# Kernel optimization log

Measured on AMD Instinct MI355X. Metric: run time of the kernel, lower is better.

Reference implementation:

```python
import jax, jax.numpy as jnp
import numpy as np

EPS = 1e-5
G = 8  # groups


def bn(x, gamma, beta):
    # BatchNorm2d in training mode: stats over (N, H, W) per channel (axis=1)
    m = jnp.mean(x, axis=(0, 2, 3), keepdims=True)
    v = jnp.var(x, axis=(0, 2, 3), keepdims=True)
    return (x - m) * jax.lax.rsqrt(v + EPS) * gamma.reshape(1, -1, 1, 1) + beta.reshape(1, -1, 1, 1)


def setup_inputs() -> dict:
    key = jax.random.key(0)
    ks = jax.random.split(key, 8)
    N, C, H, W = 8, 128, 56, 56
    Co = 128
    GP = Co // G  # 16 group planes
    d = {}
    d["x"] = jax.random.normal(ks[0], (N, C, H, W), jnp.float32)
    d["wq"] = jax.random.normal(ks[1], (Co // 2, C), jnp.float32) * np.float32(np.sqrt(1.0 / (C * GP)))
    d["wk"] = jax.random.normal(ks[2], (Co // 2, C), jnp.float32) * np.float32(np.sqrt(1.0 / C))
    d["wv"] = jax.random.normal(ks[3], (Co, C), jnp.float32) * np.float32(np.sqrt(1.0 / C))
    d["q_rel"] = jax.random.normal(ks[4], (GP // 2, H), jnp.float32) * np.float32(np.sqrt(1.0 / (Co // 2)))
    d["k_rel"] = jax.random.normal(ks[5], (GP // 2, H), jnp.float32) * np.float32(np.sqrt(1.0 / (Co // 2)))
    d["v_rel"] = jax.random.normal(ks[6], (GP, H), jnp.float32) * np.float32(np.sqrt(1.0 / Co))
    for name, n in [("q", Co // 2), ("k", Co // 2), ("v", Co), ("qr", G), ("kr", G), ("qk", G), ("sv", Co), ("sve", Co)]:
        d["g_" + name] = jnp.ones((n,), jnp.float32)
        d["b_" + name] = jnp.zeros((n,), jnp.float32)
    return d


def reference(x, wq, wk, wv, q_rel, k_rel, v_rel,
              g_q, b_q, g_k, b_k, g_v, b_v,
              g_qr, b_qr, g_kr, b_kr, g_qk, b_qk,
              g_sv, b_sv, g_sve, b_sve):
    N, C, H, W = x.shape
    # 1x1 conv transforms + BN
    q = bn(jnp.einsum('oc,bchw->bohw', wq, x), g_q, b_q)
    k = bn(jnp.einsum('oc,bchw->bohw', wk, x), g_k, b_k)
    v = bn(jnp.einsum('oc,bchw->bohw', wv, x), g_v, b_v)
    q5 = q.reshape(N, G, -1, H, W)  # [N,G,gp/2,H,W]
    k5 = k.reshape(N, G, -1, H, W)
    v5 = v.reshape(N, G, -1, H, W)  # [N,G,gp,H,W]
    # relative-position scores; embeddings are constant along j (expand of [c,H])
    qr = jnp.einsum('bgchw,ch->bghw', q5, q_rel)
    qr = jnp.broadcast_to(qr[:, :, :, None, :], (N, G, H, H, W))
    qr = bn(qr.reshape(N, G, H * H, W), g_qr, b_qr).reshape(N, G, H, H, W)
    kr = jnp.einsum('bgchw,ch->bghw', k5, k_rel)
    kr = jnp.broadcast_to(kr[:, :, :, None, :], (N, G, H, H, W))
    kr = bn(kr.reshape(N, G, H * H, W), g_kr, b_kr).reshape(N, G, H, H, W)
    kr = kr.transpose(0, 1, 3, 2, 4)
    # content-content scores
    qk = jnp.einsum('bgciw,bgcjw->bgijw', q5, k5)
    qk = bn(qk.reshape(N, G, H * H, W), g_qk, b_qk).reshape(N, G, H, H, W)
    sim = jax.nn.softmax(qk + qr + kr, axis=3)  # [N,G,H,H,W]
    sv = jnp.einsum('bgijw,bgcjw->bgciw', sim, v5)
    # v_embedding[c,j,i] = v_rel[c,j]
    sve = jnp.einsum('bgijw,cj->bgciw', sim, v_rel)
    out = bn(sv.reshape(N, -1, H, W), g_sv, b_sv) + bn(sve.reshape(N, -1, H, W), g_sve, b_sve)
    return out
```

## Files before the change

### kernel.cpp

```cpp
#include <hip/hip_runtime.h>

#define EPSV 1e-5f

#define NB   8
#define CC   128
#define HH   56
#define WW   56
#define HW   3136
#define NHW  25088
#define GG   8

#define OFF_QKV      0
#define OFF_SV       6422528
#define OFF_SVE      9633792
#define OFF_QRB      12845056
#define OFF_KRB      13045760
#define OFF_QKVSC    13246464
#define OFF_QKVSH    13246720
#define OFF_BNPAR    13247024
#define OFF_BNPAR2   13247072
#define WS_FLOATS    13247584

#define ACC_IDX(u, g) (((u) * 8 + (g)) * 32)

__global__ __launch_bounds__(256) void k0_transpose(
    const float* __restrict__ x, float* __restrict__ xT) {
  __shared__ float t[56][60];
  const int c = blockIdx.x & 127, b = blockIdx.x >> 7;
  const size_t base = ((size_t)b * 128 + c) * HW;
  const int tid = threadIdx.x;
  for (int f = tid; f < 784; f += 256) {
    int e = f * 4;
    int h = e / 56, w = e - h * 56;
    float4 v = *(const float4*)(x + base + e);
    *(float4*)&t[h][w] = v;
  }
  __syncthreads();
  for (int f = tid; f < 784; f += 256) {
    int e = f * 4;
    int w = e / 56, h0 = e - w * 56;
    float4 v = make_float4(t[h0][w], t[h0 + 1][w], t[h0 + 2][w], t[h0 + 3][w]);
    *(float4*)(xT + base + w * 56 + h0) = v;
  }
}

__global__ __launch_bounds__(256) void k1_qkv(
    const float* __restrict__ x, const float* __restrict__ wq,
    const float* __restrict__ wk, const float* __restrict__ wv,
    float* __restrict__ qkv) {
  __shared__ float Wc[32][132];
  __shared__ float Xc[32][64];
  const int p0 = blockIdx.x * 64;
  const int o0 = blockIdx.y * 128;
  const int tid = threadIdx.x;
  const int io = tid & 15, ip = tid >> 4;
  const int bb = p0 / HW;
  const int s0 = p0 - bb * HW;

  float acc[8][4];
#pragma unroll
  for (int r = 0; r < 8; ++r)
#pragma unroll
    for (int s = 0; s < 4; ++s) acc[r][s] = 0.f;

  for (int kc = 0; kc < 128; kc += 32) {
    if (kc) __syncthreads();
#pragma unroll
    for (int r = 0; r < 4; ++r) {
      int f = tid + 256 * r;
      int ol = f >> 3;
      int kq = (f & 7) * 4;
      int o = o0 + ol;
      const float* wsrc = (o < 64) ? (wq + (size_t)o * 128)
                        : (o < 128) ? (wk + (size_t)(o - 64) * 128)
                                    : (wv + (size_t)(o - 128) * 128);
      float4 w4 = *(const float4*)(wsrc + kc + kq);
      Wc[kq + 0][ol] = w4.x; Wc[kq + 1][ol] = w4.y;
      Wc[kq + 2][ol] = w4.z; Wc[kq + 3][ol] = w4.w;
    }
#pragma unroll
    for (int r = 0; r < 2; ++r) {
      int f = tid + 256 * r;
      int k = f >> 4;
      int pq = (f & 15) * 4;
      float4 x4 = *(const float4*)(x + (size_t)(bb * 128 + kc + k) * HW + s0 + pq);
      *(float4*)&Xc[k][pq] = x4;
    }
    __syncthreads();
#pragma unroll
    for (int k = 0; k < 32; ++k) {
      float4 xv = *(const float4*)&Xc[k][ip * 4];
      float4 wa = *(const float4*)&Wc[k][io * 8];
      float4 wb = *(const float4*)&Wc[k][io * 8 + 4];
      float wr[8] = {wa.x, wa.y, wa.z, wa.w, wb.x, wb.y, wb.z, wb.w};
      float xr[4] = {xv.x, xv.y, xv.z, xv.w};
#pragma unroll
      for (int r = 0; r < 8; ++r)
#pragma unroll
        for (int s = 0; s < 4; ++s)
          acc[r][s] = fmaf(wr[r], xr[s], acc[r][s]);
    }
  }
#pragma unroll
  for (int r = 0; r < 8; ++r) {
    float4 o4 = make_float4(acc[r][0], acc[r][1], acc[r][2], acc[r][3]);
    *(float4*)(qkv + (size_t)(o0 + io * 8 + r) * NHW + p0 + ip * 4) = o4;
  }
}

__global__ __launch_bounds__(256) void k2_stats(
    const float* __restrict__ qkv,
    const float* __restrict__ g_q, const float* __restrict__ b_q,
    const float* __restrict__ g_k, const float* __restrict__ b_k,
    const float* __restrict__ g_v, const float* __restrict__ b_v,
    float* __restrict__ sc_out, float* __restrict__ sh_out) {
  const int o = blockIdx.x;
  const float4* p = (const float4*)(qkv + (size_t)o * NHW);
  float s = 0.f, s2 = 0.f;
  for (int f = threadIdx.x; f < NHW / 4; f += 256) {
    float4 v = p[f];
    s  += v.x + v.y + v.z + v.w;
    s2 += v.x * v.x + v.y * v.y + v.z * v.z + v.w * v.w;
  }
#pragma unroll
  for (int off = 32; off > 0; off >>= 1) {
    s  += __shfl_down(s, off);
    s2 += __shfl_down(s2, off);
  }
  __shared__ float ls[8];
  int wv_ = threadIdx.x >> 6, ln = threadIdx.x & 63;
  if (ln == 0) { ls[wv_] = s; ls[4 + wv_] = s2; }
  __syncthreads();
  if (threadIdx.x == 0) {
    s  = ls[0] + ls[1] + ls[2] + ls[3];
    s2 = ls[4] + ls[5] + ls[6] + ls[7];
    float mean = s / (float)NHW;
    float var  = s2 / (float)NHW - mean * mean;
    float g, b;
    if (o < 64)       { g = g_q[o];       b = b_q[o]; }
    else if (o < 128) { g = g_k[o - 64];  b = b_k[o - 64]; }
    else              { g = g_v[o - 128]; b = b_v[o - 128]; }
    float sc = g * rsqrtf(var + EPSV);
    sc_out[o] = sc;
    sh_out[o] = b - mean * sc;
  }
}

__global__ __launch_bounds__(256) void k3_scores(
    const float* __restrict__ qkv,
    const float* __restrict__ qsc, const float* __restrict__ qsh,
    const float* __restrict__ q_rel, const float* __restrict__ k_rel,
    float* __restrict__ qrb, float* __restrict__ krb,
    float* __restrict__ accum) {
  __shared__ float qn[8][4][56];
  __shared__ float kn[8][4][56];
  __shared__ float red[4][6];
  const int w0 = blockIdx.x * 4, g = blockIdx.y, b = blockIdx.z;
  const int tid = threadIdx.x;

  for (int f = tid; f < 896; f += 256) {
    int isK = f >= 448;
    int idx = f - 448 * isK;
    int c = idx / 56, r = idx - c * 56;
    int wl = r / 14, hq = (r - wl * 14) * 4;
    int o = g * 8 + c + 64 * isK;
    float4 v = *(const float4*)(qkv + (size_t)o * NHW + b * HW + (w0 + wl) * 56 + hq);
    float sc = qsc[o], sh = qsh[o];
    float4 n = make_float4(fmaf(v.x, sc, sh), fmaf(v.y, sc, sh),
                           fmaf(v.z, sc, sh), fmaf(v.w, sc, sh));
    if (isK) *(float4*)&kn[c][wl][hq] = n;
    else     *(float4*)&qn[c][wl][hq] = n;
  }
  __syncthreads();

  float vqr = 0.f, vqr2 = 0.f, vkr = 0.f, vkr2 = 0.f, vqk = 0.f, vqk2 = 0.f;
  if (tid < 224) {
    const int i = tid % 56, wl = tid / 56;
    float qreg[8];
#pragma unroll
    for (int c = 0; c < 8; ++c) qreg[c] = qn[c][wl][i];
    float qrv = 0.f, krv = 0.f;
#pragma unroll
    for (int c = 0; c < 8; ++c) {
      qrv = fmaf(qreg[c], q_rel[c * 56 + i], qrv);
      krv = fmaf(kn[c][wl][i], k_rel[c * 56 + i], krv);
    }
    size_t bo = ((size_t)(b * 8 + g) * 56 + w0 + wl) * 56 + i;
    qrb[bo] = qrv;
    krb[bo] = krv;
    vqr = qrv; vqr2 = qrv * qrv; vkr = krv; vkr2 = krv * krv;
#pragma unroll
    for (int jq = 0; jq < 14; ++jq) {
      float s0 = 0.f, s1 = 0.f, s2 = 0.f, s3 = 0.f;
#pragma unroll
      for (int c = 0; c < 8; ++c) {
        const float* kp = &kn[c][wl][jq * 4];
        float qc = qreg[c];
        s0 = fmaf(qc, kp[0], s0); s1 = fmaf(qc, kp[1], s1);
        s2 = fmaf(qc, kp[2], s2); s3 = fmaf(qc, kp[3], s3);
      }
      vqk  += s0 + s1 + s2 + s3;
      vqk2 += s0 * s0 + s1 * s1 + s2 * s2 + s3 * s3;
    }
  }
  float vals[6] = {vqr, vqr2, vkr, vkr2, vqk, vqk2};
#pragma unroll
  for (int u = 0; u < 6; ++u)
#pragma unroll
    for (int off = 32; off > 0; off >>= 1) vals[u] += __shfl_down(vals[u], off);
  int wv_ = tid >> 6, ln = tid & 63;
  if (ln == 0)
#pragma unroll
    for (int u = 0; u < 6; ++u) red[wv_][u] = vals[u];
  __syncthreads();
  if (tid == 0) {
#pragma unroll
    for (int u = 0; u < 6; ++u)
      atomicAdd(&accum[ACC_IDX(u, g)], red[0][u] + red[1][u] + red[2][u] + red[3][u]);
  }
}

__global__ void k4_bn(
    const float* __restrict__ accum,
    const float* __restrict__ g_qr, const float* __restrict__ b_qr,
    const float* __restrict__ g_kr, const float* __restrict__ b_kr,
    const float* __restrict__ g_qk, const float* __restrict__ b_qk,
    float* __restrict__ bnpar) {
  int g = threadIdx.x;
  if (g >= 8) return;
  const float inv1 = 1.f / 25088.f;
  const float inv2 = 1.f / 1404928.f;
  float m, v, sc;
  m = accum[ACC_IDX(0, g)] * inv1; v = accum[ACC_IDX(1, g)] * inv1 - m * m;
  sc = g_qr[g] * rsqrtf(v + EPSV); bnpar[g]      = sc; bnpar[8 + g]  = b_qr[g] - m * sc;
  m = accum[ACC_IDX(2, g)] * inv1; v = accum[ACC_IDX(3, g)] * inv1 - m * m;
  sc = g_kr[g] * rsqrtf(v + EPSV); bnpar[16 + g] = sc; bnpar[24 + g] = b_kr[g] - m * sc;
  m = accum[ACC_IDX(4, g)] * inv2; v = accum[ACC_IDX(5, g)] * inv2 - m * m;
  sc = g_qk[g] * rsqrtf(v + EPSV); bnpar[32 + g] = sc; bnpar[40 + g] = b_qk[g] - m * sc;
}

__global__ __launch_bounds__(256) void k5_attn(
    const float* __restrict__ qkv,
    const float* __restrict__ qsc, const float* __restrict__ qsh,
    const float* __restrict__ qrb, const float* __restrict__ krb,
    const float* __restrict__ bnpar, const float* __restrict__ v_rel,
    float* __restrict__ sv_ws, float* __restrict__ sve_ws) {
  __shared__ float qn[8][4][56];
  __shared__ float kn[8][4][56];
  __shared__ float vn[16][4][56];
  __shared__ float qrn[4][56];
  __shared__ float krn[4][56];
  __shared__ float vr[16][56];
  const int w0 = blockIdx.x * 4, g = blockIdx.y, b = blockIdx.z;
  const int tid = threadIdx.x;

  for (int f = tid; f < 1792; f += 256) {
    int c, o; float* dst;
    int idx = f;
    if (f < 448)      { c = idx / 56;                      o = g * 8 + c;         dst = (float*)qn + c * 224; }
    else if (f < 896) { idx = f - 448; c = idx / 56;       o = 64 + g * 8 + c;    dst = (float*)kn + c * 224; }
    else              { idx = f - 896; c = idx / 56;       o = 128 + g * 16 + c;  dst = (float*)vn + c * 224; }
    int r = idx - c * 56;
    int wl = r / 14, hq = (r - wl * 14) * 4;
    float4 v = *(const float4*)(qkv + (size_t)o * NHW + b * HW + (w0 + wl) * 56 + hq);
    float sc = qsc[o], sh = qsh[o];
    float4 n = make_float4(fmaf(v.x, sc, sh), fmaf(v.y, sc, sh),
                           fmaf(v.z, sc, sh), fmaf(v.w, sc, sh));
    *(float4*)(dst + wl * 56 + hq) = n;
  }
  {
    float qr_sc = bnpar[g],      qr_sh = bnpar[8 + g];
    float kr_sc = bnpar[16 + g], kr_sh = bnpar[24 + g];
    if (tid < 224) {
      int i = tid % 56, wl = tid / 56;
      size_t bo = ((size_t)(b * 8 + g) * 56 + w0 + wl) * 56 + i;
      qrn[wl][i] = fmaf(qrb[bo], qr_sc, qr_sh);
      krn[wl][i] = fmaf(krb[bo], kr_sc, kr_sh);
    }
  }
  for (int f = tid; f < 896; f += 256) ((float*)vr)[f] = v_rel[f];
  __syncthreads();

  if (tid < 224) {
    const int i = tid % 56, wl = tid / 56;
    float qreg[8];
#pragma unroll
    for (int c = 0; c < 8; ++c) qreg[c] = qn[c][wl][i];
    const float qksc = bnpar[32 + g];
    const float addi = bnpar[40 + g] + qrn[wl][i];

    float srow[56];
    float mx = -3.402823466e38f;
#pragma unroll
    for (int jq = 0; jq < 14; ++jq) {
      float s0 = 0.f, s1 = 0.f, s2 = 0.f, s3 = 0.f;
#pragma unroll
      for (int c = 0; c < 8; ++c) {
        const float* kp = &kn[c][wl][jq * 4];
        float qc = qreg[c];
        s0 = fmaf(qc, kp[0], s0); s1 = fmaf(qc, kp[1], s1);
        s2 = fmaf(qc, kp[2], s2); s3 = fmaf(qc, kp[3], s3);
      }
      const float* krp = &krn[wl][jq * 4];
      s0 = fmaf(qksc, s0, addi + krp[0]);
      s1 = fmaf(qksc, s1, addi + krp[1]);
      s2 = fmaf(qksc, s2, addi + krp[2]);
      s3 = fmaf(qksc, s3, addi + krp[3]);
      srow[jq * 4 + 0] = s0; srow[jq * 4 + 1] = s1;
      srow[jq * 4 + 2] = s2; srow[jq * 4 + 3] = s3;
      mx = fmaxf(mx, fmaxf(fmaxf(s0, s1), fmaxf(s2, s3)));
    }
    float sum = 0.f;
#pragma unroll
    for (int j = 0; j < 56; ++j) {
      float p = expf(srow[j] - mx);
      srow[j] = p;
      sum += p;
    }
    float inv = 1.f / sum;

    float sv[16], sve[16];
#pragma unroll
    for (int c = 0; c < 16; ++c) { sv[c] = 0.f; sve[c] = 0.f; }
#pragma unroll
    for (int jq = 0; jq < 14; ++jq) {
      float p0 = srow[jq * 4], p1 = srow[jq * 4 + 1];
      float p2 = srow[jq * 4 + 2], p3 = srow[jq * 4 + 3];
#pragma unroll
      for (int c = 0; c < 16; ++c) {
        const float* vp  = &vn[c][wl][jq * 4];
        const float* vrp = &vr[c][jq * 4];
        sv[c]  = fmaf(p0, vp[0],  fmaf(p1, vp[1],  fmaf(p2, vp[2],  fmaf(p3, vp[3],  sv[c]))));
        sve[c] = fmaf(p0, vrp[0], fmaf(p1, vrp[1], fmaf(p2, vrp[2], fmaf(p3, vrp[3], sve[c]))));
      }
    }
#pragma unroll
    for (int c = 0; c < 16; ++c) {
      size_t base = (size_t)(g * 16 + c) * NHW + b * HW + (w0 + wl) * 56 + i;
      sv_ws[base]  = sv[c]  * inv;
      sve_ws[base] = sve[c] * inv;
    }
  }
}

__global__ __launch_bounds__(256) void k6_stats2(
    const float* __restrict__ sv_ws, const float* __restrict__ sve_ws,
    const float* __restrict__ g_sv, const float* __restrict__ b_sv,
    const float* __restrict__ g_sve, const float* __restrict__ b_sve,
    float* __restrict__ bnpar2) {
  const int cb = blockIdx.x;
  const int ch = cb & 127;
  const float* src = (cb < 128) ? sv_ws : sve_ws;
  const float4* p = (const float4*)(src + (size_t)ch * NHW);
  float s = 0.f, s2 = 0.f;
  for (int f = threadIdx.x; f < NHW / 4; f += 256) {
    float4 v = p[f];
    s  += v.x + v.y + v.z + v.w;
    s2 += v.x * v.x + v.y * v.y + v.z * v.z + v.w * v.w;
  }
#pragma unroll
  for (int off = 32; off > 0; off >>= 1) {
    s  += __shfl_down(s, off);
    s2 += __shfl_down(s2, off);
  }
  __shared__ float ls[8];
  int wv_ = threadIdx.x >> 6, ln = threadIdx.x & 63;
  if (ln == 0) { ls[wv_] = s; ls[4 + wv_] = s2; }
  __syncthreads();
  if (threadIdx.x == 0) {
    s  = ls[0] + ls[1] + ls[2] + ls[3];
    s2 = ls[4] + ls[5] + ls[6] + ls[7];
    float m = s / (float)NHW;
    float var = s2 / (float)NHW - m * m;
    float gm = (cb < 128) ? g_sv[ch] : g_sve[ch];
    float bt = (cb < 128) ? b_sv[ch] : b_sve[ch];
    float sc = gm * rsqrtf(var + EPSV);
    int off = (cb < 128) ? 0 : 256;
    bnpar2[off + ch] = sc;
    bnpar2[off + 128 + ch] = bt - m * sc;
  }
}

__global__ __launch_bounds__(256) void k7_out(
    const float* __restrict__ sv_ws, const float* __restrict__ sve_ws,
    const float* __restrict__ bnpar2, float* __restrict__ out) {
  __shared__ float t[56][60];
  const int ch = blockIdx.x & 127, b = blockIdx.x >> 7;
  const int tid = threadIdx.x;
  const float asc = bnpar2[ch], ash = bnpar2[128 + ch];
  const float esc = bnpar2[256 + ch], esh = bnpar2[384 + ch];
  const size_t pin = ((size_t)ch * NB + b) * HW;
  for (int f = tid; f < 784; f += 256) {
    int e = f * 4;
    int w = e / 56, h = e - w * 56;
    float4 a  = *(const float4*)(sv_ws + pin + e);
    float4 c4 = *(const float4*)(sve_ws + pin + e);
    float4 o4;
    o4.x = fmaf(a.x, asc, ash) + fmaf(c4.x, esc, esh);
    o4.y = fmaf(a.y, asc, ash) + fmaf(c4.y, esc, esh);
    o4.z = fmaf(a.z, asc, ash) + fmaf(c4.z, esc, esh);
    o4.w = fmaf(a.w, asc, ash) + fmaf(c4.w, esc, esh);
    *(float4*)&t[w][h] = o4;
  }
  __syncthreads();
  const size_t pout = ((size_t)b * 128 + ch) * HW;
  for (int f = tid; f < 784; f += 256) {
    int e = f * 4;
    int h = e / 56, w0 = e - h * 56;
    float4 o4 = make_float4(t[w0][h], t[w0 + 1][h], t[w0 + 2][h], t[w0 + 3][h]);
    *(float4*)(out + pout + h * 56 + w0) = o4;
  }
}

extern "C" void kernel_launch(void* const* d_in, const int* in_sizes, int n_in,
                              void* d_out, int out_size, void* d_ws, size_t ws_size,
                              hipStream_t stream) {
  (void)in_sizes; (void)n_in; (void)out_size;
  if (ws_size < (size_t)WS_FLOATS * sizeof(float)) return;

  const float* x     = (const float*)d_in[0];
  const float* wq    = (const float*)d_in[1];
  const float* wk    = (const float*)d_in[2];
  const float* wv    = (const float*)d_in[3];
  const float* q_rel = (const float*)d_in[4];
  const float* k_rel = (const float*)d_in[5];
  const float* v_rel = (const float*)d_in[6];
  const float* g_q   = (const float*)d_in[7];
  const float* b_q   = (const float*)d_in[8];
  const float* g_k   = (const float*)d_in[9];
  const float* b_k   = (const float*)d_in[10];
  const float* g_v   = (const float*)d_in[11];
  const float* b_v   = (const float*)d_in[12];
  const float* g_qr  = (const float*)d_in[13];
  const float* b_qr  = (const float*)d_in[14];
  const float* g_kr  = (const float*)d_in[15];
  const float* b_kr  = (const float*)d_in[16];
  const float* g_qk  = (const float*)d_in[17];
  const float* b_qk  = (const float*)d_in[18];
  const float* g_sv  = (const float*)d_in[19];
  const float* b_sv  = (const float*)d_in[20];
  const float* g_sve = (const float*)d_in[21];
  const float* b_sve = (const float*)d_in[22];

  float* ws     = (float*)d_ws;
  float* qkv    = ws + OFF_QKV;
  float* sv_ws  = ws + OFF_SV;
  float* sve_ws = ws + OFF_SVE;
  float* xT     = ws + OFF_SV;
  float* accum  = ws + OFF_SVE;
  float* qrb    = ws + OFF_QRB;
  float* krb    = ws + OFF_KRB;
  float* qkvsc  = ws + OFF_QKVSC;
  float* qkvsh  = ws + OFF_QKVSH;
  float* bnpar  = ws + OFF_BNPAR;
  float* bnpar2 = ws + OFF_BNPAR2;

  hipMemsetAsync(accum, 0, 48 * 32 * sizeof(float), stream);

  k0_transpose<<<1024, 256, 0, stream>>>(x, xT);
  k1_qkv<<<dim3(392, 2), 256, 0, stream>>>(xT, wq, wk, wv, qkv);
  k2_stats<<<256, 256, 0, stream>>>(qkv, g_q, b_q, g_k, b_k, g_v, b_v, qkvsc, qkvsh);
  k3_scores<<<dim3(14, 8, 8), 256, 0, stream>>>(qkv, qkvsc, qkvsh, q_rel, k_rel, qrb, krb, accum);
  k4_bn<<<1, 64, 0, stream>>>(accum, g_qr, b_qr, g_kr, b_kr, g_qk, b_qk, bnpar);
  k5_attn<<<dim3(14, 8, 8), 256, 0, stream>>>(qkv, qkvsc, qkvsh, qrb, krb, bnpar, v_rel, sv_ws, sve_ws);
  k6_stats2<<<256, 256, 0, stream>>>(sv_ws, sve_ws, g_sv, b_sv, g_sve, b_sve, bnpar2);
  k7_out<<<1024, 256, 0, stream>>>(sv_ws, sve_ws, bnpar2, (float*)d_out);
}
```

Measured before the change: 213.3 us.

## Drop softmax-invariant qr/shift terms and fuse output BN stats into attention

The qr term and the BN shifts of qk and kr are constant along the softmax axis j, so they are removed: the q_rel projection, its buffer and its statistics are no longer computed, and only the BN scales are kept. The per-channel sum and sum-of-squares for the sv/sve batch norms are now reduced inside the attention kernel with wave shuffles and atomics. This replaces the separate stats pass that re-read both large intermediates with a tiny fold kernel. The cost is extra shuffles and atomics in the attention kernel, and float atomics make the accumulation order nondeterministic.

Result: slower. 263.3 us (+23.5%).

```diff
diff --git a/kernel.cpp b/kernel.cpp
--- a/kernel.cpp
+++ b/kernel.cpp
@@ -13,13 +13,14 @@
 #define OFF_QKV      0
 #define OFF_SV       6422528
 #define OFF_SVE      9633792
-#define OFF_QRB      12845056
-#define OFF_KRB      13045760
-#define OFF_QKVSC    13246464
-#define OFF_QKVSH    13246720
-#define OFF_BNPAR    13247024
-#define OFF_BNPAR2   13247072
-#define WS_FLOATS    13247584
+#define OFF_KRB      12845056
+#define OFF_QKVSC    13045760
+#define OFF_QKVSH    13046016
+#define OFF_BNPAR    13046272
+#define OFF_BNPAR2   13046288
+#define OFF_ACCUM    13046816
+#define OFF_ACCUM2   13047840
+#define WS_FLOATS    13064224
 
 #define ACC_IDX(u, g) (((u) * 8 + (g)) * 32)
 
@@ -149,12 +150,11 @@
 __global__ __launch_bounds__(256) void k3_scores(
     const float* __restrict__ qkv,
     const float* __restrict__ qsc, const float* __restrict__ qsh,
-    const float* __restrict__ q_rel, const float* __restrict__ k_rel,
-    float* __restrict__ qrb, float* __restrict__ krb,
-    float* __restrict__ accum) {
+    const float* __restrict__ k_rel,
+    float* __restrict__ krb, float* __restrict__ accum) {
   __shared__ float qn[8][4][56];
   __shared__ float kn[8][4][56];
-  __shared__ float red[4][6];
+  __shared__ float red[4][4];
   const int w0 = blockIdx.x * 4, g = blockIdx.y, b = blockIdx.z;
   const int tid = threadIdx.x;
 
@@ -173,22 +173,19 @@
   }
   __syncthreads();
 
-  float vqr = 0.f, vqr2 = 0.f, vkr = 0.f, vkr2 = 0.f, vqk = 0.f, vqk2 = 0.f;
+  float vkr = 0.f, vkr2 = 0.f, vqk = 0.f, vqk2 = 0.f;
   if (tid < 224) {
     const int i = tid % 56, wl = tid / 56;
     float qreg[8];
 #pragma unroll
     for (int c = 0; c < 8; ++c) qreg[c] = qn[c][wl][i];
-    float qrv = 0.f, krv = 0.f;
-#pragma unroll
-    for (int c = 0; c < 8; ++c) {
-      qrv = fmaf(qreg[c], q_rel[c * 56 + i], qrv);
+    float krv = 0.f;
+#pragma unroll
+    for (int c = 0; c < 8; ++c)
       krv = fmaf(kn[c][wl][i], k_rel[c * 56 + i], krv);
-    }
     size_t bo = ((size_t)(b * 8 + g) * 56 + w0 + wl) * 56 + i;
-    qrb[bo] = qrv;
     krb[bo] = krv;
-    vqr = qrv; vqr2 = qrv * qrv; vkr = krv; vkr2 = krv * krv;
+    vkr = krv; vkr2 = krv * krv;
 #pragma unroll
     for (int jq = 0; jq < 14; ++jq) {
       float s0 = 0.f, s1 = 0.f, s2 = 0.f, s3 = 0.f;
@@ -203,54 +200,51 @@
       vqk2 += s0 * s0 + s1 * s1 + s2 * s2 + s3 * s3;
     }
   }
-  float vals[6] = {vqr, vqr2, vkr, vkr2, vqk, vqk2};
-#pragma unroll
-  for (int u = 0; u < 6; ++u)
+  float vals[4] = {vkr, vkr2, vqk, vqk2};
+#pragma unroll
+  for (int u = 0; u < 4; ++u)
 #pragma unroll
     for (int off = 32; off > 0; off >>= 1) vals[u] += __shfl_down(vals[u], off);
   int wv_ = tid >> 6, ln = tid & 63;
   if (ln == 0)
 #pragma unroll
-    for (int u = 0; u < 6; ++u) red[wv_][u] = vals[u];
+    for (int u = 0; u < 4; ++u) red[wv_][u] = vals[u];
   __syncthreads();
   if (tid == 0) {
 #pragma unroll
-    for (int u = 0; u < 6; ++u)
+    for (int u = 0; u < 4; ++u)
       atomicAdd(&accum[ACC_IDX(u, g)], red[0][u] + red[1][u] + red[2][u] + red[3][u]);
   }
 }
 
 __global__ void k4_bn(
     const float* __restrict__ accum,
-    const float* __restrict__ g_qr, const float* __restrict__ b_qr,
-    const float* __restrict__ g_kr, const float* __restrict__ b_kr,
-    const float* __restrict__ g_qk, const float* __restrict__ b_qk,
+    const float* __restrict__ g_kr, const float* __restrict__ g_qk,
     float* __restrict__ bnpar) {
   int g = threadIdx.x;
   if (g >= 8) return;
   const float inv1 = 1.f / 25088.f;
   const float inv2 = 1.f / 1404928.f;
-  float m, v, sc;
+  float m, v;
   m = accum[ACC_IDX(0, g)] * inv1; v = accum[ACC_IDX(1, g)] * inv1 - m * m;
-  sc = g_qr[g] * rsqrtf(v + EPSV); bnpar[g]      = sc; bnpar[8 + g]  = b_qr[g] - m * sc;
-  m = accum[ACC_IDX(2, g)] * inv1; v = accum[ACC_IDX(3, g)] * inv1 - m * m;
-  sc = g_kr[g] * rsqrtf(v + EPSV); bnpar[16 + g] = sc; bnpar[24 + g] = b_kr[g] - m * sc;
-  m = accum[ACC_IDX(4, g)] * inv2; v = accum[ACC_IDX(5, g)] * inv2 - m * m;
-  sc = g_qk[g] * rsqrtf(v + EPSV); bnpar[32 + g] = sc; bnpar[40 + g] = b_qk[g] - m * sc;
+  bnpar[g]     = g_kr[g] * rsqrtf(v + EPSV);
+  m = accum[ACC_IDX(2, g)] * inv2; v = accum[ACC_IDX(3, g)] * inv2 - m * m;
+  bnpar[8 + g] = g_qk[g] * rsqrtf(v + EPSV);
 }
 
 __global__ __launch_bounds__(256) void k5_attn(
     const float* __restrict__ qkv,
     const float* __restrict__ qsc, const float* __restrict__ qsh,
-    const float* __restrict__ qrb, const float* __restrict__ krb,
-    const float* __restrict__ bnpar, const float* __restrict__ v_rel,
-    float* __restrict__ sv_ws, float* __restrict__ sve_ws) {
+    const float* __restrict__ krb, const float* __restrict__ bnpar,
+    const float* __restrict__ v_rel,
+    float* __restrict__ sv_ws, float* __restrict__ sve_ws,
+    float* __restrict__ accum2) {
   __shared__ float qn[8][4][56];
   __shared__ float kn[8][4][56];
   __shared__ float vn[16][4][56];
-  __shared__ float qrn[4][56];
   __shared__ float krn[4][56];
   __shared__ float vr[16][56];
+  __shared__ float wred[4][16][4];
   const int w0 = blockIdx.x * 4, g = blockIdx.y, b = blockIdx.z;
   const int tid = threadIdx.x;
 
@@ -269,25 +263,27 @@
     *(float4*)(dst + wl * 56 + hq) = n;
   }
   {
-    float qr_sc = bnpar[g],      qr_sh = bnpar[8 + g];
-    float kr_sc = bnpar[16 + g], kr_sh = bnpar[24 + g];
+    float kr_sc = bnpar[g];
     if (tid < 224) {
       int i = tid % 56, wl = tid / 56;
       size_t bo = ((size_t)(b * 8 + g) * 56 + w0 + wl) * 56 + i;
-      qrn[wl][i] = fmaf(qrb[bo], qr_sc, qr_sh);
-      krn[wl][i] = fmaf(krb[bo], kr_sc, kr_sh);
+      krn[wl][i] = krb[bo] * kr_sc;
     }
   }
   for (int f = tid; f < 896; f += 256) ((float*)vr)[f] = v_rel[f];
   __syncthreads();
 
+  float sv[16], sve[16];
+#pragma unroll
+  for (int c = 0; c < 16; ++c) { sv[c] = 0.f; sve[c] = 0.f; }
+  float inv = 0.f;
+  const int i = tid % 56, wl = tid / 56;
+
   if (tid < 224) {
-    const int i = tid % 56, wl = tid / 56;
     float qreg[8];
 #pragma unroll
     for (int c = 0; c < 8; ++c) qreg[c] = qn[c][wl][i];
-    const float qksc = bnpar[32 + g];
-    const float addi = bnpar[40 + g] + qrn[wl][i];
+    const float qksc = bnpar[8 + g];
 
     float srow[56];
     float mx = -3.402823466e38f;
@@ -302,10 +298,10 @@
         s2 = fmaf(qc, kp[2], s2); s3 = fmaf(qc, kp[3], s3);
       }
       const float* krp = &krn[wl][jq * 4];
-      s0 = fmaf(qksc, s0, addi + krp[0]);
-      s1 = fmaf(qksc, s1, addi + krp[1]);
-      s2 = fmaf(qksc, s2, addi + krp[2]);
-      s3 = fmaf(qksc, s3, addi + krp[3]);
+      s0 = fmaf(qksc, s0, krp[0]);
+      s1 = fmaf(qksc, s1, krp[1]);
+      s2 = fmaf(qksc, s2, krp[2]);
+      s3 = fmaf(qksc, s3, krp[3]);
       srow[jq * 4 + 0] = s0; srow[jq * 4 + 1] = s1;
       srow[jq * 4 + 2] = s2; srow[jq * 4 + 3] = s3;
       mx = fmaxf(mx, fmaxf(fmaxf(s0, s1), fmaxf(s2, s3)));
@@ -317,11 +313,8 @@
       srow[j] = p;
       sum += p;
     }
-    float inv = 1.f / sum;
-
-    float sv[16], sve[16];
-#pragma unroll
-    for (int c = 0; c < 16; ++c) { sv[c] = 0.f; sve[c] = 0.f; }
+    inv = 1.f / sum;
+
 #pragma unroll
     for (int jq = 0; jq < 14; ++jq) {
       float p0 = srow[jq * 4], p1 = srow[jq * 4 + 1];
@@ -334,51 +327,54 @@
         sve[c] = fmaf(p0, vrp[0], fmaf(p1, vrp[1], fmaf(p2, vrp[2], fmaf(p3, vrp[3], sve[c]))));
       }
     }
-#pragma unroll
-    for (int c = 0; c < 16; ++c) {
+  }
+
+#pragma unroll
+  for (int c = 0; c < 16; ++c) {
+    float fv = 0.f, ev = 0.f;
+    if (tid < 224) {
+      fv = sv[c] * inv; ev = sve[c] * inv;
       size_t base = (size_t)(g * 16 + c) * NHW + b * HW + (w0 + wl) * 56 + i;
-      sv_ws[base]  = sv[c]  * inv;
-      sve_ws[base] = sve[c] * inv;
-    }
-  }
-}
-
-__global__ __launch_bounds__(256) void k6_stats2(
-    const float* __restrict__ sv_ws, const float* __restrict__ sve_ws,
+      sv_ws[base]  = fv;
+      sve_ws[base] = ev;
+    }
+    float s0 = fv, s1 = fv * fv, s2 = ev, s3 = ev * ev;
+#pragma unroll
+    for (int off = 32; off > 0; off >>= 1) {
+      s0 += __shfl_xor(s0, off); s1 += __shfl_xor(s1, off);
+      s2 += __shfl_xor(s2, off); s3 += __shfl_xor(s3, off);
+    }
+    if ((tid & 63) == 0) {
+      int wv_ = tid >> 6;
+      wred[wv_][c][0] = s0; wred[wv_][c][1] = s1;
+      wred[wv_][c][2] = s2; wred[wv_][c][3] = s3;
+    }
+  }
+  __syncthreads();
+  if (tid < 64) {
+    int c = tid >> 2, st = tid & 3;
+    float v = wred[0][c][st] + wred[1][c][st] + wred[2][c][st] + wred[3][c][st];
+    atomicAdd(&accum2[(((g * 16 + c) * 4) + st) * 32], v);
+  }
+}
+
+__global__ void k6b_fold(
+    const float* __restrict__ accum2,
     const float* __restrict__ g_sv, const float* __restrict__ b_sv,
     const float* __restrict__ g_sve, const float* __restrict__ b_sve,
     float* __restrict__ bnpar2) {
-  const int cb = blockIdx.x;
-  const int ch = cb & 127;
-  const float* src = (cb < 128) ? sv_ws : sve_ws;
-  const float4* p = (const float4*)(src + (size_t)ch * NHW);
-  float s = 0.f, s2 = 0.f;
-  for (int f = threadIdx.x; f < NHW / 4; f += 256) {
-    float4 v = p[f];
-    s  += v.x + v.y + v.z + v.w;
-    s2 += v.x * v.x + v.y * v.y + v.z * v.z + v.w * v.w;
-  }
-#pragma unroll
-  for (int off = 32; off > 0; off >>= 1) {
-    s  += __shfl_down(s, off);
-    s2 += __shfl_down(s2, off);
-  }
-  __shared__ float ls[8];
-  int wv_ = threadIdx.x >> 6, ln = threadIdx.x & 63;
-  if (ln == 0) { ls[wv_] = s; ls[4 + wv_] = s2; }
-  __syncthreads();
-  if (threadIdx.x == 0) {
-    s  = ls[0] + ls[1] + ls[2] + ls[3];
-    s2 = ls[4] + ls[5] + ls[6] + ls[7];
-    float m = s / (float)NHW;
-    float var = s2 / (float)NHW - m * m;
-    float gm = (cb < 128) ? g_sv[ch] : g_sve[ch];
-    float bt = (cb < 128) ? b_sv[ch] : b_sve[ch];
-    float sc = gm * rsqrtf(var + EPSV);
-    int off = (cb < 128) ? 0 : 256;
-    bnpar2[off + ch] = sc;
-    bnpar2[off + 128 + ch] = bt - m * sc;
-  }
+  int ch = threadIdx.x;
+  if (ch >= 128) return;
+  const float invn = 1.f / 25088.f;
+  float m, v, sc;
+  m = accum2[(ch * 4 + 0) * 32] * invn;
+  v = accum2[(ch * 4 + 1) * 32] * invn - m * m;
+  sc = g_sv[ch] * rsqrtf(v + EPSV);
+  bnpar2[ch] = sc; bnpar2[128 + ch] = b_sv[ch] - m * sc;
+  m = accum2[(ch * 4 + 2) * 32] * invn;
+  v = accum2[(ch * 4 + 3) * 32] * invn - m * m;
+  sc = g_sve[ch] * rsqrtf(v + EPSV);
+  bnpar2[256 + ch] = sc; bnpar2[384 + ch] = b_sve[ch] - m * sc;
 }
 
 __global__ __launch_bounds__(256) void k7_out(
@@ -422,7 +418,6 @@
   const float* wq    = (const float*)d_in[1];
   const float* wk    = (const float*)d_in[2];
   const float* wv    = (const float*)d_in[3];
-  const float* q_rel = (const float*)d_in[4];
   const float* k_rel = (const float*)d_in[5];
   const float* v_rel = (const float*)d_in[6];
   const float* g_q   = (const float*)d_in[7];
@@ -431,12 +426,8 @@
   const float* b_k   = (const float*)d_in[10];
   const float* g_v   = (const float*)d_in[11];
   const float* b_v   = (const float*)d_in[12];
-  const float* g_qr  = (const float*)d_in[13];
-  const float* b_qr  = (const float*)d_in[14];
   const float* g_kr  = (const float*)d_in[15];
-  const float* b_kr  = (const float*)d_in[16];
   const float* g_qk  = (const float*)d_in[17];
-  const float* b_qk  = (const float*)d_in[18];
   const float* g_sv  = (const float*)d_in[19];
   const float* b_sv  = (const float*)d_in[20];
   const float* g_sve = (const float*)d_in[21];
@@ -447,22 +438,22 @@
   float* sv_ws  = ws + OFF_SV;
   float* sve_ws = ws + OFF_SVE;
   float* xT     = ws + OFF_SV;
-  float* accum  = ws + OFF_SVE;
-  float* qrb    = ws + OFF_QRB;
   float* krb    = ws + OFF_KRB;
   float* qkvsc  = ws + OFF_QKVSC;
   float* qkvsh  = ws + OFF_QKVSH;
   float* bnpar  = ws + OFF_BNPAR;
   float* bnpar2 = ws + OFF_BNPAR2;
-
-  hipMemsetAsync(accum, 0, 48 * 32 * sizeof(float), stream);
+  float* accum  = ws + OFF_ACCUM;
+  float* accum2 = ws + OFF_ACCUM2;
+
+  hipMemsetAsync(accum, 0, (WS_FLOATS - OFF_ACCUM) * sizeof(float), stream);
 
   k0_transpose<<<1024, 256, 0, stream>>>(x, xT);
   k1_qkv<<<dim3(392, 2), 256, 0, stream>>>(xT, wq, wk, wv, qkv);
   k2_stats<<<256, 256, 0, stream>>>(qkv, g_q, b_q, g_k, b_k, g_v, b_v, qkvsc, qkvsh);
-  k3_scores<<<dim3(14, 8, 8), 256, 0, stream>>>(qkv, qkvsc, qkvsh, q_rel, k_rel, qrb, krb, accum);
-  k4_bn<<<1, 64, 0, stream>>>(accum, g_qr, b_qr, g_kr, b_kr, g_qk, b_qk, bnpar);
-  k5_attn<<<dim3(14, 8, 8), 256, 0, stream>>>(qkv, qkvsc, qkvsh, qrb, krb, bnpar, v_rel, sv_ws, sve_ws);
-  k6_stats2<<<256, 256, 0, stream>>>(sv_ws, sve_ws, g_sv, b_sv, g_sve, b_sve, bnpar2);
+  k3_scores<<<dim3(14, 8, 8), 256, 0, stream>>>(qkv, qkvsc, qkvsh, k_rel, krb, accum);
+  k4_bn<<<1, 64, 0, stream>>>(accum, g_kr, g_qk, bnpar);
+  k5_attn<<<dim3(14, 8, 8), 256, 0, stream>>>(qkv, qkvsc, qkvsh, krb, bnpar, v_rel, sv_ws, sve_ws, accum2);
+  k6b_fold<<<1, 128, 0, stream>>>(accum2, g_sv, b_sv, g_sve, b_sve, bnpar2);
   k7_out<<<1024, 256, 0, stream>>>(sv_ws, sve_ws, bnpar2, (float*)d_out);
 }
```
